# Kernel tuning notes

Hardware: AMD Instinct MI355X
Metric: run time of the kernel (lower is better)

The kernel has to match this reference:

```python
import jax, jax.numpy as jnp
import numpy as np

B, T, V, C, K = 256, 2048, 128, 512, 10


def setup_inputs() -> dict:
    key = jax.random.key(0)
    k0, k1, k2, k3 = jax.random.split(key, 4)
    x = jax.random.normal(k0, (B, C), dtype=jnp.float32)
    # kappa_old: running attention position, non-negative, somewhere in [0, T)
    kappa_old = jax.random.uniform(k1, (B, K), dtype=jnp.float32) * T
    # onehots: one-hot encoded text, (B, T, V)
    char_ids = jax.random.randint(k2, (B, T), 0, V)
    onehots = jax.nn.one_hot(char_ids, V, dtype=jnp.float32)
    # Linear(cell_size, 3*K) params; torch stores weight as (out, in)
    W = jax.random.normal(k3, (3 * K, C), dtype=jnp.float32) * 0.02
    b = jnp.zeros((3 * K,), dtype=jnp.float32)
    return {"x": x, "kappa_old": kappa_old, "onehots": onehots, "W": W, "b": b}


def reference(x, kappa_old, onehots, W, b):
    max_text_len = onehots.shape[1]
    params = jnp.exp(x @ W.T + b)                      # (B, 3K)
    alpha, beta, pre_kappa = jnp.split(params, 3, axis=-1)  # each (B, K)
    kappa = kappa_old + pre_kappa                      # (B, K)
    indices = jnp.arange(max_text_len, dtype=x.dtype)  # (T,)
    # gravity: (B, K, T) via broadcast, then exp + alpha-weighted reduce over K
    gravity = -beta[:, :, None] * (kappa[:, :, None] - indices) ** 2
    phi = jnp.einsum("bk,bkt->bt", alpha, jnp.exp(gravity))  # (B, T)
    w = jnp.einsum("bt,btv->bv", phi, onehots)               # (B, V)
    return (w, kappa, phi)
```

## Files before the change

kernel.cpp:

```cpp
#include <hip/hip_runtime.h>

#define B_ 256
#define T_ 2048
#define V_ 128
#define C_ 512
#define K_ 10

#define W_OFF 0
#define KAPPA_OFF (B_ * V_)
#define PHI_OFF   (B_ * V_ + B_ * K_)

#define EPS 1e-7f

#define NG 32
#define RPG (T_ / NG)

typedef float f4_t __attribute__((ext_vector_type(4)));

__global__ __launch_bounds__(1024) void window_fused(
    const float* __restrict__ x, const float* __restrict__ kappa_old,
    const float* __restrict__ W, const float* __restrict__ bias,
    const float* __restrict__ onehots, float* __restrict__ out) {
  const int b = blockIdx.x;
  const int tid = threadIdx.x;

  __shared__ f4_t xs4[C_ / 4];
  __shared__ float alpha_s[K_];
  __shared__ float beta_s[K_];
  __shared__ float kap_s[K_];
  __shared__ float phs[T_];
  __shared__ float red[NG * V_];

  if (tid < C_ / 4) xs4[tid] = ((const f4_t*)(x + b * C_))[tid];
  __syncthreads();

  const int j = tid >> 5;
  const int l = tid & 31;
  if (j < 3 * K_) {
    const f4_t* Wr = (const f4_t*)(W + j * C_);
    f4_t a4 = {0.f, 0.f, 0.f, 0.f};
#pragma unroll
    for (int m = 0; m < 4; ++m) a4 += Wr[m * 32 + l] * xs4[m * 32 + l];
    float acc = (a4.x + a4.y) + (a4.z + a4.w);
    acc += __shfl_down(acc, 16, 32);
    acc += __shfl_down(acc, 8, 32);
    acc += __shfl_down(acc, 4, 32);
    acc += __shfl_down(acc, 2, 32);
    acc += __shfl_down(acc, 1, 32);
    if (l == 0) {
      const float p = __expf(acc + bias[j]);
      if (j < K_) {
        alpha_s[j] = p;
      } else if (j < 2 * K_) {
        beta_s[j - K_] = p;
      } else {
        const int k = j - 2 * K_;
        const float kk = kappa_old[b * K_ + k] + p;
        kap_s[k] = kk;
        out[KAPPA_OFF + b * K_ + k] = kk;
      }
    }
  }
  __syncthreads();

#pragma unroll
  for (int half = 0; half < 2; ++half) {
    const int t = tid + half * 1024;
    const float ft = (float)t;
    float ph = 0.0f;
#pragma unroll
    for (int k = 0; k < K_; k++) {
      const float d = kap_s[k] - ft;
      ph += alpha_s[k] * __expf(-beta_s[k] * d * d);
    }
    phs[t] = ph;
    out[PHI_OFF + b * T_ + t] = ph;
  }
  __syncthreads();

  const int g = tid >> 5;
  const int vg = tid & 31;
  const f4_t* p0 =
      (const f4_t*)(onehots + ((size_t)b * T_ + g) * V_) + vg;

  unsigned long long mask = 0;
#pragma unroll 8
  for (int jj = 0; jj < RPG; ++jj)
    if (phs[g + 32 * jj] >= EPS) mask |= 1ull << jj;

  f4_t acc = {0.f, 0.f, 0.f, 0.f};
  int j0 = -1, j1 = -1, j2 = -1, j3 = -1;
  f4_t o0 = acc, o1 = acc, o2 = acc, o3 = acc;
  if (mask) { j0 = __builtin_ctzll(mask); mask &= mask - 1;
              o0 = __builtin_nontemporal_load(p0 + (size_t)j0 * 1024); }
  if (mask) { j1 = __builtin_ctzll(mask); mask &= mask - 1;
              o1 = __builtin_nontemporal_load(p0 + (size_t)j1 * 1024); }
  if (mask) { j2 = __builtin_ctzll(mask); mask &= mask - 1;
              o2 = __builtin_nontemporal_load(p0 + (size_t)j2 * 1024); }
  if (mask) { j3 = __builtin_ctzll(mask); mask &= mask - 1;
              o3 = __builtin_nontemporal_load(p0 + (size_t)j3 * 1024); }
  while (j0 >= 0) {
    acc += phs[g + 32 * j0] * o0;
    j0 = j1; o0 = o1;
    j1 = j2; o1 = o2;
    j2 = j3; o2 = o3;
    if (mask) { j3 = __builtin_ctzll(mask); mask &= mask - 1;
                o3 = __builtin_nontemporal_load(p0 + (size_t)j3 * 1024); }
    else j3 = -1;
  }

  *(f4_t*)&red[g * V_ + vg * 4] = acc;
  __syncthreads();

  if (tid < V_) {
    float s0 = 0.0f;
#pragma unroll
    for (int r = 0; r < NG; r++) s0 += red[r * V_ + tid];
    out[W_OFF + b * V_ + tid] = s0;
  }
}

extern "C" void kernel_launch(void* const* d_in, const int* in_sizes, int n_in,
                              void* d_out, int out_size, void* d_ws,
                              size_t ws_size, hipStream_t stream) {
  const float* x         = (const float*)d_in[0];
  const float* kappa_old = (const float*)d_in[1];
  const float* onehots   = (const float*)d_in[2];
  const float* W         = (const float*)d_in[3];
  const float* bias      = (const float*)d_in[4];
  float* out = (float*)d_out;

  window_fused<<<dim3(B_), dim3(1024), 0, stream>>>(x, kappa_old, W, bias,
                                                    onehots, out);
}
```

Baseline: 307.2 us.

## Predict active onehot rows analytically and prefetch them before phi computation

Instead of building the row mask from computed phi values, the kernel now derives, per mixture component, the interval of t where alpha*exp(-beta*d^2) can exceed about 1e-8. It builds the mask from these intervals with wave ballots and issues the first onehot loads before computing phi, so memory latency overlaps the exp work. It also hoists the W, bias and kappa_old loads ahead of the first barrier and makes the phi stores nontemporal. The analytic interval is a per-component bound, so rows whose phi is a sum of several small components could be classified slightly differently from the old phi>=eps test.

```diff
diff --git a/kernel.cpp b/kernel.cpp
--- a/kernel.cpp
+++ b/kernel.cpp
@@ -23,24 +23,36 @@
     const float* __restrict__ onehots, float* __restrict__ out) {
   const int b = blockIdx.x;
   const int tid = threadIdx.x;
+  const int j = tid >> 5;
+  const int l = tid & 31;
 
   __shared__ f4_t xs4[C_ / 4];
   __shared__ float alpha_s[K_];
   __shared__ float beta_s[K_];
   __shared__ float kap_s[K_];
+  __shared__ float lo_s[K_];
+  __shared__ float hi_s[K_];
   __shared__ float phs[T_];
   __shared__ float red[NG * V_];
 
+  f4_t w4[4];
+  float bj = 0.0f, ko = 0.0f;
+  if (j < 3 * K_) {
+    const f4_t* Wr = (const f4_t*)(W + j * C_);
+#pragma unroll
+    for (int m = 0; m < 4; ++m) w4[m] = Wr[m * 32 + l];
+    if (l == 0) {
+      bj = bias[j];
+      if (j >= 2 * K_) ko = kappa_old[b * K_ + (j - 2 * K_)];
+    }
+  }
   if (tid < C_ / 4) xs4[tid] = ((const f4_t*)(x + b * C_))[tid];
   __syncthreads();
 
-  const int j = tid >> 5;
-  const int l = tid & 31;
   if (j < 3 * K_) {
-    const f4_t* Wr = (const f4_t*)(W + j * C_);
     f4_t a4 = {0.f, 0.f, 0.f, 0.f};
 #pragma unroll
-    for (int m = 0; m < 4; ++m) a4 += Wr[m * 32 + l] * xs4[m * 32 + l];
+    for (int m = 0; m < 4; ++m) a4 += w4[m] * xs4[m * 32 + l];
     float acc = (a4.x + a4.y) + (a4.z + a4.w);
     acc += __shfl_down(acc, 16, 32);
     acc += __shfl_down(acc, 8, 32);
@@ -48,20 +60,61 @@
     acc += __shfl_down(acc, 2, 32);
     acc += __shfl_down(acc, 1, 32);
     if (l == 0) {
-      const float p = __expf(acc + bias[j]);
+      const float p = __expf(acc + bj);
       if (j < K_) {
         alpha_s[j] = p;
       } else if (j < 2 * K_) {
         beta_s[j - K_] = p;
       } else {
         const int k = j - 2 * K_;
-        const float kk = kappa_old[b * K_ + k] + p;
+        const float kk = ko + p;
         kap_s[k] = kk;
         out[KAPPA_OFF + b * K_ + k] = kk;
       }
     }
   }
   __syncthreads();
+
+  if (tid < K_) {
+    const float L = __logf(alpha_s[tid] * 1e8f);
+    const float r = (L > 0.f) ? sqrtf(L / beta_s[tid]) : -1.0f;
+    lo_s[tid] = kap_s[tid] - r;
+    hi_s[tid] = kap_s[tid] + r;
+  }
+  __syncthreads();
+
+  const float t0f = (float)(j + 32 * l);
+  const float t1f = t0f + 1024.0f;
+  bool act0 = false, act1 = false;
+#pragma unroll
+  for (int k = 0; k < K_; ++k) {
+    const float lo = lo_s[k], hi = hi_s[k];
+    act0 |= (t0f >= lo) & (t0f <= hi);
+    act1 |= (t1f >= lo) & (t1f <= hi);
+  }
+  const unsigned long long ba0 = __ballot(act0);
+  const unsigned long long ba1 = __ballot(act1);
+  const unsigned int m0 =
+      (j & 1) ? (unsigned int)(ba0 >> 32) : (unsigned int)ba0;
+  const unsigned int m1 =
+      (j & 1) ? (unsigned int)(ba1 >> 32) : (unsigned int)ba1;
+  unsigned long long mask =
+      (unsigned long long)m0 | ((unsigned long long)m1 << 32);
+
+  const f4_t* p0 =
+      (const f4_t*)(onehots + ((size_t)b * T_ + j) * V_) + l;
+
+  f4_t acc4 = {0.f, 0.f, 0.f, 0.f};
+  int j0 = -1, j1 = -1, j2 = -1, j3 = -1;
+  f4_t o0 = acc4, o1 = acc4, o2 = acc4, o3 = acc4;
+  if (mask) { j0 = __builtin_ctzll(mask); mask &= mask - 1;
+              o0 = __builtin_nontemporal_load(p0 + (size_t)j0 * 1024); }
+  if (mask) { j1 = __builtin_ctzll(mask); mask &= mask - 1;
+              o1 = __builtin_nontemporal_load(p0 + (size_t)j1 * 1024); }
+  if (mask) { j2 = __builtin_ctzll(mask); mask &= mask - 1;
+              o2 = __builtin_nontemporal_load(p0 + (size_t)j2 * 1024); }
+  if (mask) { j3 = __builtin_ctzll(mask); mask &= mask - 1;
+              o3 = __builtin_nontemporal_load(p0 + (size_t)j3 * 1024); }
 
 #pragma unroll
   for (int half = 0; half < 2; ++half) {
@@ -74,33 +127,12 @@
       ph += alpha_s[k] * __expf(-beta_s[k] * d * d);
     }
     phs[t] = ph;
-    out[PHI_OFF + b * T_ + t] = ph;
+    __builtin_nontemporal_store(ph, out + PHI_OFF + b * T_ + t);
   }
   __syncthreads();
 
-  const int g = tid >> 5;
-  const int vg = tid & 31;
-  const f4_t* p0 =
-      (const f4_t*)(onehots + ((size_t)b * T_ + g) * V_) + vg;
-
-  unsigned long long mask = 0;
-#pragma unroll 8
-  for (int jj = 0; jj < RPG; ++jj)
-    if (phs[g + 32 * jj] >= EPS) mask |= 1ull << jj;
-
-  f4_t acc = {0.f, 0.f, 0.f, 0.f};
-  int j0 = -1, j1 = -1, j2 = -1, j3 = -1;
-  f4_t o0 = acc, o1 = acc, o2 = acc, o3 = acc;
-  if (mask) { j0 = __builtin_ctzll(mask); mask &= mask - 1;
-              o0 = __builtin_nontemporal_load(p0 + (size_t)j0 * 1024); }
-  if (mask) { j1 = __builtin_ctzll(mask); mask &= mask - 1;
-              o1 = __builtin_nontemporal_load(p0 + (size_t)j1 * 1024); }
-  if (mask) { j2 = __builtin_ctzll(mask); mask &= mask - 1;
-              o2 = __builtin_nontemporal_load(p0 + (size_t)j2 * 1024); }
-  if (mask) { j3 = __builtin_ctzll(mask); mask &= mask - 1;
-              o3 = __builtin_nontemporal_load(p0 + (size_t)j3 * 1024); }
   while (j0 >= 0) {
-    acc += phs[g + 32 * j0] * o0;
+    acc4 += phs[j + 32 * j0] * o0;
     j0 = j1; o0 = o1;
     j1 = j2; o1 = o2;
     j2 = j3; o2 = o3;
@@ -109,7 +141,7 @@
     else j3 = -1;
   }
 
-  *(f4_t*)&red[g * V_ + vg * 4] = acc;
+  *(f4_t*)&red[j * V_ + l * 4] = acc4;
   __syncthreads();
 
   if (tid < V_) {
```

After: 301.0 us. 1.02x faster.
